# Optimization experiments

Measured on AMD Instinct MI355X. Metric: run time of the kernel, lower is better.

The kernel has to match this reference:

```python
import jax, jax.numpy as jnp
import numpy as np

N = 100000    # nodes
E = 800000    # directed edges
EF = 16       # edge features
NF = 1        # node features (forced by the module's MLP-size constraint)
HID = NF * 8  # NNConv out = 8
H1, C1 = 8, 16  # gat1 heads / per-head channels -> 128
NC = 16       # num_classes (gat2: heads=1, out=NC)


def setup_inputs() -> dict:
    key = jax.random.key(0)
    ks = jax.random.split(key, 20)
    s = 0.1
    return {
        "x": jax.random.normal(ks[0], (N, NF), jnp.float32),
        "edge_index": jax.random.randint(ks[1], (2, E), 0, N, jnp.int64),
        "edge_attr": jax.random.normal(ks[2], (E, EF), jnp.float32),
        # edge MLP: Linear(EF,8) -> ReLU -> Linear(8,8)
        "w1": jax.random.normal(ks[3], (EF, HID), jnp.float32) * s,
        "b1": jnp.zeros((HID,), jnp.float32),
        "w2": jax.random.normal(ks[4], (HID, HID), jnp.float32) * s,
        "b2": jnp.zeros((HID,), jnp.float32),
        # NNConv root weight + bias
        "root": jax.random.normal(ks[5], (NF, HID), jnp.float32) * s,
        "nn_bias": jnp.zeros((HID,), jnp.float32),
        # GAT1: in 8 -> 16 ch x 8 heads
        "g1W": jax.random.normal(ks[6], (HID, H1 * C1), jnp.float32) * s,
        "g1as": jax.random.normal(ks[7], (H1, C1), jnp.float32) * s,
        "g1ad": jax.random.normal(ks[8], (H1, C1), jnp.float32) * s,
        "g1b": jnp.zeros((H1 * C1,), jnp.float32),
        # GAT2: in 128 -> NC, 1 head
        "g2W": jax.random.normal(ks[9], (H1 * C1, NC), jnp.float32) * s,
        "g2as": jax.random.normal(ks[10], (1, NC), jnp.float32) * s,
        "g2ad": jax.random.normal(ks[11], (1, NC), jnp.float32) * s,
        "g2b": jnp.zeros((NC,), jnp.float32),
    }


def _gat(h_in, W, a_src, a_dst, bias, src, dst, n, heads, ch):
    # h: [N, heads, ch]
    h = (h_in @ W).reshape(n, heads, ch)
    e_s = jnp.einsum("nhc,hc->nh", h, a_src)   # per-node src logits
    e_d = jnp.einsum("nhc,hc->nh", h, a_dst)
    e = jax.nn.leaky_relu(e_s[src] + e_d[dst], 0.2)      # [E2, heads]
    m = jax.ops.segment_max(e, dst, num_segments=n)      # segment softmax
    e = jnp.exp(e - m[dst])
    z = jax.ops.segment_sum(e, dst, num_segments=n)
    alpha = e / (z[dst] + 1e-16)                          # [E2, heads]
    out = jax.ops.segment_sum(alpha[:, :, None] * h[src], dst, num_segments=n)
    return out.reshape(n, heads * ch) + bias


def reference(x, edge_index, edge_attr, w1, b1, w2, b2, root, nn_bias,
              g1W, g1as, g1ad, g1b, g2W, g2as, g2ad, g2b):
    n = x.shape[0]
    src, dst = edge_index[0], edge_index[1]

    # ---- NNConv (aggr='mean'): per-edge weight from edge MLP ----
    w_e = jax.nn.relu(edge_attr @ w1 + b1) @ w2 + b2      # [E, NF*HID]
    w_e = w_e.reshape(-1, NF, HID)
    msg = jnp.einsum("ei,eio->eo", x[src], w_e)            # [E, HID]
    sums = jax.ops.segment_sum(msg, dst, num_segments=n)
    cnt = jax.ops.segment_sum(jnp.ones((msg.shape[0],), msg.dtype), dst, num_segments=n)
    aggr = sums / jnp.maximum(cnt, 1.0)[:, None]
    h = jax.nn.relu(aggr + x @ root + nn_bias)             # [N, 8]
    # dropout: eval mode -> identity

    # ---- add self-loops (PyG GATConv default) ----
    loops = jnp.arange(n, dtype=src.dtype)
    src2 = jnp.concatenate([src, loops])
    dst2 = jnp.concatenate([dst, loops])

    h = jax.nn.elu(_gat(h, g1W, g1as, g1ad, g1b, src2, dst2, n, H1, C1))  # [N,128]
    out = _gat(h, g2W, g2as, g2ad, g2b, src2, dst2, n, 1, NC)             # [N,16]
    return jax.nn.log_softmax(out, axis=1)
```

## Files before the change

kernel.cpp:

```cpp
#include <hip/hip_runtime.h>
#include <hip/hip_fp16.h>
#include <math.h>

constexpr int NN  = 100000;
constexpr int NE  = 800000;
constexpr int H1 = 8, C1 = 16;
constexpr int D1 = H1 * C1;
constexpr int NC = 16;
constexpr int SCAN_B = 256;
constexpr int SCAN_NB = (NN + SCAN_B - 1) / SCAN_B;

static inline int cdiv(int a, int b) { return (a + b - 1) / b; }

typedef int   v4i __attribute__((ext_vector_type(4)));

__device__ inline __half2 h2_bits(unsigned u) {
    __half2 r; __builtin_memcpy(&r, &u, 4); return r;
}
__device__ inline __half2 shflx_h2(__half2 v, int off) {
    int iv; __builtin_memcpy(&iv, &v, 4);
    iv = __shfl_xor(iv, off);
    __half2 r; __builtin_memcpy(&r, &iv, 4); return r;
}

__global__ void hist_kernel(const int* __restrict__ dst, int* __restrict__ deg) {
    int e = blockIdx.x * blockDim.x + threadIdx.x;
    if (e < NE) atomicAdd(&deg[dst[e]], 1);
}

__global__ void scan1(const int* __restrict__ deg, int* __restrict__ row,
                      int* __restrict__ partial) {
    __shared__ int s[SCAN_B];
    int tid = threadIdx.x;
    int i = blockIdx.x * SCAN_B + tid;
    int v = (i < NN) ? deg[i] : 0;
    s[tid] = v;
    __syncthreads();
    for (int off = 1; off < SCAN_B; off <<= 1) {
        int t = 0;
        if (tid >= off) t = s[tid - off];
        __syncthreads();
        s[tid] += t;
        __syncthreads();
    }
    if (i < NN) row[i] = s[tid] - v;
    if (tid == SCAN_B - 1) partial[blockIdx.x] = s[tid];
}

__global__ void scan2(int* __restrict__ partial, int nb) {
    __shared__ int s[512];
    int tid = threadIdx.x;
    int v = (tid < nb) ? partial[tid] : 0;
    s[tid] = v;
    __syncthreads();
    for (int off = 1; off < 512; off <<= 1) {
        int t = 0;
        if (tid >= off) t = s[tid - off];
        __syncthreads();
        s[tid] += t;
        __syncthreads();
    }
    if (tid < nb) partial[tid] = s[tid] - v;
}

__global__ void scan3(int* __restrict__ row, const int* __restrict__ partial,
                      int* __restrict__ cursor) {
    int i = blockIdx.x * SCAN_B + threadIdx.x;
    if (i < NN) {
        int r = row[i] + partial[blockIdx.x];
        row[i] = r;
        cursor[i] = r;
    }
}

__global__ void nnconv_scatter(const float* __restrict__ x,
                               const int* __restrict__ src, const int* __restrict__ dst,
                               const float* __restrict__ ea,
                               const float* __restrict__ w1, const float* __restrict__ b1,
                               const float* __restrict__ w2, const float* __restrict__ b2,
                               int* __restrict__ cursor,
                               int* __restrict__ src_s, int* __restrict__ eid_s,
                               __half* __restrict__ msg_s) {
    __shared__ float sw1[16 * 8], sw2[8 * 8], sb1[8], sb2[8];
    int t = threadIdx.x;
    if (t < 128) sw1[t] = w1[t];
    else if (t < 192) sw2[t - 128] = w2[t - 128];
    else if (t < 200) sb1[t - 192] = b1[t - 192];
    else if (t < 208) sb2[t - 200] = b2[t - 200];
    __syncthreads();
    int e = blockIdx.x * blockDim.x + t;
    if (e >= NE) return;

    float a[16];
    const float4* ea4 = (const float4*)(ea + (size_t)e * 16);
    float4 v0 = ea4[0], v1 = ea4[1], v2 = ea4[2], v3 = ea4[3];
    a[0]=v0.x; a[1]=v0.y; a[2]=v0.z; a[3]=v0.w;
    a[4]=v1.x; a[5]=v1.y; a[6]=v1.z; a[7]=v1.w;
    a[8]=v2.x; a[9]=v2.y; a[10]=v2.z; a[11]=v2.w;
    a[12]=v3.x; a[13]=v3.y; a[14]=v3.z; a[15]=v3.w;

    float hdn[8];
#pragma unroll
    for (int j = 0; j < 8; j++) {
        float s = sb1[j];
#pragma unroll
        for (int i = 0; i < 16; i++) s = fmaf(a[i], sw1[i * 8 + j], s);
        hdn[j] = fmaxf(s, 0.f);
    }
    int sn = src[e], dn = dst[e];
    float xv = x[sn];
    __align__(16) __half msg[8];
#pragma unroll
    for (int j = 0; j < 8; j++) {
        float s = sb2[j];
#pragma unroll
        for (int i = 0; i < 8; i++) s = fmaf(hdn[i], sw2[i * 8 + j], s);
        msg[j] = __float2half(xv * s);
    }
    v4i mv; __builtin_memcpy(&mv, msg, 16);
    __builtin_nontemporal_store(mv, (v4i*)(msg_s + (size_t)e * 8));
    int pos = atomicAdd(&cursor[dn], 1);
    src_s[pos] = sn;
    eid_s[pos] = e;
}

__global__ void fused_node1(const float* __restrict__ x,
                            const int* __restrict__ row, const int* __restrict__ deg,
                            const int* __restrict__ eid_s,
                            const __half* __restrict__ msg_s,
                            const float* __restrict__ root, const float* __restrict__ nb,
                            const float* __restrict__ W,
                            const float* __restrict__ as_, const float* __restrict__ ad_,
                            __half* __restrict__ h1h,
                            float* __restrict__ es, float* __restrict__ ed) {
    int t = blockIdx.x * blockDim.x + threadIdx.x;
    if (t >= NN * 8) return;
    int n = t >> 3, j = t & 7;
    int rs = row[n], d = deg[n];

    float p0 = 0.f, p1 = 0.f, p2 = 0.f, p3 = 0.f;
    float p4 = 0.f, p5 = 0.f, p6 = 0.f, p7 = 0.f;
    for (int k = j; k < d; k += 8) {
        int eid = eid_s[rs + k];
        uint4 m = *(const uint4*)(msg_s + (size_t)eid * 8);
        float2 f0 = __half22float2(h2_bits(m.x));
        float2 f1 = __half22float2(h2_bits(m.y));
        float2 f2 = __half22float2(h2_bits(m.z));
        float2 f3 = __half22float2(h2_bits(m.w));
        p0 += f0.x; p1 += f0.y; p2 += f1.x; p3 += f1.y;
        p4 += f2.x; p5 += f2.y; p6 += f3.x; p7 += f3.y;
    }
    float k0 = (j & 4) ? p4 : p0, s0 = (j & 4) ? p0 : p4;
    float k1 = (j & 4) ? p5 : p1, s1 = (j & 4) ? p1 : p5;
    float k2 = (j & 4) ? p6 : p2, s2 = (j & 4) ? p2 : p6;
    float k3 = (j & 4) ? p7 : p3, s3 = (j & 4) ? p3 : p7;
    k0 += __shfl_xor(s0, 4); k1 += __shfl_xor(s1, 4);
    k2 += __shfl_xor(s2, 4); k3 += __shfl_xor(s3, 4);
    float m0 = (j & 2) ? k2 : k0, n0 = (j & 2) ? k0 : k2;
    float m1 = (j & 2) ? k3 : k1, n1 = (j & 2) ? k1 : k3;
    m0 += __shfl_xor(n0, 2); m1 += __shfl_xor(n1, 2);
    float q  = (j & 1) ? m1 : m0, r = (j & 1) ? m0 : m1;
    float sum = q + __shfl_xor(r, 1);

    float hj = fmaxf(sum / fmaxf((float)d, 1.f) + x[n] * root[j] + nb[j], 0.f);

    float hv[8];
#pragma unroll
    for (int k = 0; k < 8; k++) hv[k] = __shfl(hj, k, 8);

    int hd = j;
    float acc[16];
#pragma unroll
    for (int c = 0; c < 16; c++) acc[c] = 0.f;
#pragma unroll
    for (int k = 0; k < 8; k++) {
        const float* wr = W + k * D1 + hd * 16;
#pragma unroll
        for (int c = 0; c < 16; c++) acc[c] = fmaf(hv[k], wr[c], acc[c]);
    }
    float s = 0.f, dd = 0.f;
    __align__(16) __half hh[16];
#pragma unroll
    for (int c = 0; c < 16; c++) {
        s = fmaf(acc[c], as_[hd * 16 + c], s);
        dd = fmaf(acc[c], ad_[hd * 16 + c], dd);
        hh[c] = __float2half(acc[c]);
    }
    float4* hp = (float4*)(h1h + (size_t)n * D1 + hd * 16);
    hp[0] = ((const float4*)hh)[0];
    hp[1] = ((const float4*)hh)[1];
    es[t] = s;
    ed[t] = dd;
}

__global__ __launch_bounds__(256) void gat1_gather(
        const int* __restrict__ row, const int* __restrict__ deg,
        const int* __restrict__ src_s,
        const float* __restrict__ es, const float* __restrict__ ed,
        const __half* __restrict__ h1h, const float* __restrict__ b,
        const float* __restrict__ W2,
        const float* __restrict__ as2, const float* __restrict__ ad2,
        __half* __restrict__ h2h, float* __restrict__ es2, float* __restrict__ ed2) {
    __shared__ float sW2[2048];
    __shared__ float so[4][4][132];
    int tid = threadIdx.x;
    for (int idx = tid; idx < 2048; idx += 256) sW2[idx] = W2[idx];
    __syncthreads();

    int wv = tid >> 6, lane = tid & 63;
    int g  = lane >> 4;
    int cl = lane & 15;
    int hd = cl >> 1;
    const uint4* h1h4 = (const uint4*)h1h;
    float4 bv0 = *((const float4*)(b + cl * 8));
    float4 bv1 = *((const float4*)(b + cl * 8 + 4));

    int base = (blockIdx.x * 4 + wv) * 4;
    for (int i = 0; i < 4; i++) {
        int node = base + i;
        int rs = row[node], d = deg[node];
        float edn = ed[node * 8 + hd];

        float vs = es[node * 8 + hd] + edn;
        vs = fmaxf(vs, 0.2f * vs);
        float a0 = (g == 0) ? __expf(vs) : 0.f;
        float z = a0;
        __half2 ap = __float2half2_rn(a0);
        uint4 gl = h1h4[(unsigned)node * 16u + (unsigned)cl];
        __half2 acc0 = __hmul2(ap, h2_bits(gl.x));
        __half2 acc1 = __hmul2(ap, h2_bits(gl.y));
        __half2 acc2 = __hmul2(ap, h2_bits(gl.z));
        __half2 acc3 = __hmul2(ap, h2_bits(gl.w));

        for (int k = g; k < d; k += 4) {
            int s = src_s[rs + k];
            float v = es[(unsigned)s * 8u + hd] + edn;
            v = fmaxf(v, 0.2f * v);
            float a = __expf(v);
            uint4 ge = h1h4[(unsigned)s * 16u + (unsigned)cl];
            __half2 a2 = __float2half2_rn(a);
            z += a;
            acc0 = __hfma2(a2, h2_bits(ge.x), acc0);
            acc1 = __hfma2(a2, h2_bits(ge.y), acc1);
            acc2 = __hfma2(a2, h2_bits(ge.z), acc2);
            acc3 = __hfma2(a2, h2_bits(ge.w), acc3);
        }
        z += __shfl_xor(z, 16); z += __shfl_xor(z, 32);
        acc0 = __hadd2(acc0, shflx_h2(acc0, 16)); acc0 = __hadd2(acc0, shflx_h2(acc0, 32));
        acc1 = __hadd2(acc1, shflx_h2(acc1, 16)); acc1 = __hadd2(acc1, shflx_h2(acc1, 32));
        acc2 = __hadd2(acc2, shflx_h2(acc2, 16)); acc2 = __hadd2(acc2, shflx_h2(acc2, 32));
        acc3 = __hadd2(acc3, shflx_h2(acc3, 16)); acc3 = __hadd2(acc3, shflx_h2(acc3, 32));

        float rz = 1.f / (z + 1e-16f);
        float2 f0 = __half22float2(acc0), f1 = __half22float2(acc1);
        float2 f2 = __half22float2(acc2), f3 = __half22float2(acc3);
        float o0 = fmaf(f0.x, rz, bv0.x), o1 = fmaf(f0.y, rz, bv0.y);
        float o2 = fmaf(f1.x, rz, bv0.z), o3 = fmaf(f1.y, rz, bv0.w);
        float o4 = fmaf(f2.x, rz, bv1.x), o5 = fmaf(f2.y, rz, bv1.y);
        float o6 = fmaf(f3.x, rz, bv1.z), o7 = fmaf(f3.y, rz, bv1.w);
        o0 = o0 > 0.f ? o0 : __expf(o0) - 1.f;
        o1 = o1 > 0.f ? o1 : __expf(o1) - 1.f;
        o2 = o2 > 0.f ? o2 : __expf(o2) - 1.f;
        o3 = o3 > 0.f ? o3 : __expf(o3) - 1.f;
        o4 = o4 > 0.f ? o4 : __expf(o4) - 1.f;
        o5 = o5 > 0.f ? o5 : __expf(o5) - 1.f;
        o6 = o6 > 0.f ? o6 : __expf(o6) - 1.f;
        o7 = o7 > 0.f ? o7 : __expf(o7) - 1.f;
        if (g == 0) {
            float4* sp = (float4*)&so[wv][i][cl * 8];
            sp[0] = make_float4(o0, o1, o2, o3);
            sp[1] = make_float4(o4, o5, o6, o7);
        }
    }
    __asm__ __volatile__("s_waitcnt lgkmcnt(0)" ::: "memory");

    int nl = lane >> 4, c = lane & 15;
    float partial = 0.f;
#pragma unroll 4
    for (int k = 0; k < 128; k += 2) {
        float2 sv = *(const float2*)&so[wv][nl][k];
        partial = fmaf(sv.x, sW2[k * 16 + c], partial);
        partial = fmaf(sv.y, sW2[(k + 1) * 16 + c], partial);
    }
    float ta = partial * as2[c], tb = partial * ad2[c];
#pragma unroll
    for (int off = 1; off < 16; off <<= 1) {
        ta += __shfl_xor(ta, off);
        tb += __shfl_xor(tb, off);
    }
    h2h[(size_t)(base + nl) * 16 + c] = __float2half(partial);
    if (c == 0) { es2[base + nl] = ta; ed2[base + nl] = tb; }
}

__global__ __launch_bounds__(256) void gat2_gather(
        const int* __restrict__ row, const int* __restrict__ deg,
        const int* __restrict__ src_s,
        const float* __restrict__ es, const float* __restrict__ ed,
        const __half* __restrict__ h2h, const float* __restrict__ b,
        float* __restrict__ out) {
    int tid = threadIdx.x;
    int wv = tid >> 6, lane = tid & 63;
    int g = lane >> 3, l = lane & 7;
    const unsigned* h2i = (const unsigned*)h2h;
    float2 bv = ((const float2*)b)[l];
    int base = (blockIdx.x * 4 + wv) * 4;
    for (int i = 0; i < 4; i++) {
        int node = base + i;
        int rs = row[node], d = deg[node];
        float edn = ed[node];
        float vs = es[node] + edn;
        vs = fmaxf(vs, 0.2f * vs);
        float a0 = (g == 0) ? __expf(vs) : 0.f;
        float z = a0;
        __half2 acc = __hmul2(__float2half2_rn(a0),
                              h2_bits(h2i[(unsigned)node * 8u + l]));

        for (int k = g; k < d; k += 8) {
            int s = src_s[rs + k];
            float v = es[s] + edn;
            v = fmaxf(v, 0.2f * v);
            float a = __expf(v);
            unsigned hraw = h2i[(unsigned)s * 8u + l];
            z += a;
            acc = __hfma2(__float2half2_rn(a), h2_bits(hraw), acc);
        }
        z += __shfl_xor(z, 8); z += __shfl_xor(z, 16); z += __shfl_xor(z, 32);
        acc = __hadd2(acc, shflx_h2(acc, 8));
        acc = __hadd2(acc, shflx_h2(acc, 16));
        acc = __hadd2(acc, shflx_h2(acc, 32));

        float rz = 1.f / (z + 1e-16f);
        float2 f = __half22float2(acc);
        float o0 = fmaf(f.x, rz, bv.x);
        float o1 = fmaf(f.y, rz, bv.y);
        float mx = fmaxf(o0, o1);
        mx = fmaxf(mx, __shfl_xor(mx, 1));
        mx = fmaxf(mx, __shfl_xor(mx, 2));
        mx = fmaxf(mx, __shfl_xor(mx, 4));
        float ss = __expf(o0 - mx) + __expf(o1 - mx);
        ss += __shfl_xor(ss, 1); ss += __shfl_xor(ss, 2); ss += __shfl_xor(ss, 4);
        float lg = mx + __logf(ss);
        if (g == 0)
            ((float2*)out)[(unsigned)node * 8u + l] = make_float2(o0 - lg, o1 - lg);
    }
}

extern "C" void kernel_launch(void* const* d_in, const int* in_sizes, int n_in,
                              void* d_out, int out_size, void* d_ws, size_t ws_size,
                              hipStream_t stream) {
    const float* x    = (const float*)d_in[0];
    const int*   ei   = (const int*)d_in[1];
    const float* ea   = (const float*)d_in[2];
    const float* w1   = (const float*)d_in[3];
    const float* b1   = (const float*)d_in[4];
    const float* w2   = (const float*)d_in[5];
    const float* b2   = (const float*)d_in[6];
    const float* root = (const float*)d_in[7];
    const float* nb   = (const float*)d_in[8];
    const float* g1W  = (const float*)d_in[9];
    const float* g1as = (const float*)d_in[10];
    const float* g1ad = (const float*)d_in[11];
    const float* g1b  = (const float*)d_in[12];
    const float* g2W  = (const float*)d_in[13];
    const float* g2as = (const float*)d_in[14];
    const float* g2ad = (const float*)d_in[15];
    const float* g2b  = (const float*)d_in[16];
    float* out = (float*)d_out;

    const int* src = ei;
    const int* dst = ei + NE;

    float* ws = (float*)d_ws;
    size_t o = 0;
    __half* msg_s  = (__half*)(ws + o); o += (size_t)NE * 4;
    __half* h1h    = (__half*)(ws + o); o += (size_t)NN * D1 / 2;
    __half* h2h    = (__half*)(ws + o); o += (size_t)NN * NC / 2;
    int*  src_s = (int*)(ws + o); o += NE;
    int*  eid_s = (int*)(ws + o); o += NE;
    int*  deg   = (int*)(ws + o); o += NN;
    int*  row   = (int*)(ws + o); o += NN;
    int*  cur   = (int*)(ws + o); o += NN;
    int*  part  = (int*)(ws + o); o += 512;
    float* es1  = ws + o; o += (size_t)NN * H1;
    float* ed1  = ws + o; o += (size_t)NN * H1;
    float* es2  = ws + o; o += NN;
    float* ed2  = ws + o; o += NN;
    (void)ws_size; (void)in_sizes; (void)n_in; (void)out_size;

    const int B = 256;

    hipMemsetAsync(deg, 0, (size_t)NN * sizeof(int), stream);
    hist_kernel<<<cdiv(NE, B), B, 0, stream>>>(dst, deg);
    scan1<<<SCAN_NB, SCAN_B, 0, stream>>>(deg, row, part);
    scan2<<<1, 512, 0, stream>>>(part, SCAN_NB);
    scan3<<<SCAN_NB, SCAN_B, 0, stream>>>(row, part, cur);

    nnconv_scatter<<<cdiv(NE, B), B, 0, stream>>>(x, src, dst, ea, w1, b1, w2, b2,
                                                  cur, src_s, eid_s, msg_s);
    fused_node1<<<cdiv(NN * 8, B), B, 0, stream>>>(x, row, deg, eid_s, msg_s, root, nb,
                                                   g1W, g1as, g1ad, h1h, es1, ed1);
    gat1_gather<<<NN / 16, B, 0, stream>>>(row, deg, src_s, es1, ed1, h1h,
                                           g1b, g2W, g2as, g2ad, h2h, es2, ed2);
    gat2_gather<<<NN / 16, B, 0, stream>>>(row, deg, src_s, es2, ed2, h2h, g2b, out);
}
```

Before: 351.1 us.

## Store GAT1 features as scaled FP8 and scatter messages directly into CSR order

The node features h1 are now stored as FP8 (pre-scaled by 16) instead of FP16, which halves the bytes each edge gather reads in gat1_gather. Accumulation there moves from half2 FMAs to fp32 FMAs. NNConv messages are now written at their sorted CSR position rather than by edge id, which removes the eid_s array and the indirect lookup in fused_node1. In exchange the features lose precision, which may hurt accuracy, and the message stores become scattered instead of coalesced.

```diff
diff --git a/kernel.cpp b/kernel.cpp
--- a/kernel.cpp
+++ b/kernel.cpp
@@ -13,6 +13,7 @@
 static inline int cdiv(int a, int b) { return (a + b - 1) / b; }
 
 typedef int   v4i __attribute__((ext_vector_type(4)));
+typedef float v2f __attribute__((ext_vector_type(2)));
 
 __device__ inline __half2 h2_bits(unsigned u) {
     __half2 r; __builtin_memcpy(&r, &u, 4); return r;
@@ -79,8 +80,7 @@
                                const float* __restrict__ w1, const float* __restrict__ b1,
                                const float* __restrict__ w2, const float* __restrict__ b2,
                                int* __restrict__ cursor,
-                               int* __restrict__ src_s, int* __restrict__ eid_s,
-                               __half* __restrict__ msg_s) {
+                               int* __restrict__ src_s, __half* __restrict__ msg_s) {
     __shared__ float sw1[16 * 8], sw2[8 * 8], sb1[8], sb2[8];
     int t = threadIdx.x;
     if (t < 128) sw1[t] = w1[t];
@@ -117,21 +117,19 @@
         for (int i = 0; i < 8; i++) s = fmaf(hdn[i], sw2[i * 8 + j], s);
         msg[j] = __float2half(xv * s);
     }
+    int pos = atomicAdd(&cursor[dn], 1);
     v4i mv; __builtin_memcpy(&mv, msg, 16);
-    __builtin_nontemporal_store(mv, (v4i*)(msg_s + (size_t)e * 8));
-    int pos = atomicAdd(&cursor[dn], 1);
+    __builtin_nontemporal_store(mv, (v4i*)(msg_s + (size_t)pos * 8));
     src_s[pos] = sn;
-    eid_s[pos] = e;
 }
 
 __global__ void fused_node1(const float* __restrict__ x,
                             const int* __restrict__ row, const int* __restrict__ deg,
-                            const int* __restrict__ eid_s,
                             const __half* __restrict__ msg_s,
                             const float* __restrict__ root, const float* __restrict__ nb,
                             const float* __restrict__ W,
                             const float* __restrict__ as_, const float* __restrict__ ad_,
-                            __half* __restrict__ h1h,
+                            unsigned char* __restrict__ h1f8,
                             float* __restrict__ es, float* __restrict__ ed) {
     int t = blockIdx.x * blockDim.x + threadIdx.x;
     if (t >= NN * 8) return;
@@ -141,8 +139,7 @@
     float p0 = 0.f, p1 = 0.f, p2 = 0.f, p3 = 0.f;
     float p4 = 0.f, p5 = 0.f, p6 = 0.f, p7 = 0.f;
     for (int k = j; k < d; k += 8) {
-        int eid = eid_s[rs + k];
-        uint4 m = *(const uint4*)(msg_s + (size_t)eid * 8);
+        uint4 m = *(const uint4*)(msg_s + (size_t)(rs + k) * 8);
         float2 f0 = __half22float2(h2_bits(m.x));
         float2 f1 = __half22float2(h2_bits(m.y));
         float2 f2 = __half22float2(h2_bits(m.z));
@@ -179,16 +176,19 @@
         for (int c = 0; c < 16; c++) acc[c] = fmaf(hv[k], wr[c], acc[c]);
     }
     float s = 0.f, dd = 0.f;
-    __align__(16) __half hh[16];
 #pragma unroll
     for (int c = 0; c < 16; c++) {
         s = fmaf(acc[c], as_[hd * 16 + c], s);
         dd = fmaf(acc[c], ad_[hd * 16 + c], dd);
-        hh[c] = __float2half(acc[c]);
-    }
-    float4* hp = (float4*)(h1h + (size_t)n * D1 + hd * 16);
-    hp[0] = ((const float4*)hh)[0];
-    hp[1] = ((const float4*)hh)[1];
+    }
+    v4i pk;
+#pragma unroll
+    for (int w = 0; w < 4; w++) {
+        int wd = __builtin_amdgcn_cvt_pk_fp8_f32(acc[4*w] * 16.f, acc[4*w+1] * 16.f, 0, false);
+        wd = __builtin_amdgcn_cvt_pk_fp8_f32(acc[4*w+2] * 16.f, acc[4*w+3] * 16.f, wd, true);
+        pk[w] = wd;
+    }
+    *(v4i*)(h1f8 + (size_t)n * 128 + hd * 16) = pk;
     es[t] = s;
     ed[t] = dd;
 }
@@ -197,7 +197,7 @@
         const int* __restrict__ row, const int* __restrict__ deg,
         const int* __restrict__ src_s,
         const float* __restrict__ es, const float* __restrict__ ed,
-        const __half* __restrict__ h1h, const float* __restrict__ b,
+        const unsigned char* __restrict__ h1f8, const float* __restrict__ b,
         const float* __restrict__ W2,
         const float* __restrict__ as2, const float* __restrict__ ad2,
         __half* __restrict__ h2h, float* __restrict__ es2, float* __restrict__ ed2) {
@@ -211,7 +211,6 @@
     int g  = lane >> 4;
     int cl = lane & 15;
     int hd = cl >> 1;
-    const uint4* h1h4 = (const uint4*)h1h;
     float4 bv0 = *((const float4*)(b + cl * 8));
     float4 bv1 = *((const float4*)(b + cl * 8 + 4));
 
@@ -225,39 +224,45 @@
         vs = fmaxf(vs, 0.2f * vs);
         float a0 = (g == 0) ? __expf(vs) : 0.f;
         float z = a0;
-        __half2 ap = __float2half2_rn(a0);
-        uint4 gl = h1h4[(unsigned)node * 16u + (unsigned)cl];
-        __half2 acc0 = __hmul2(ap, h2_bits(gl.x));
-        __half2 acc1 = __hmul2(ap, h2_bits(gl.y));
-        __half2 acc2 = __hmul2(ap, h2_bits(gl.z));
-        __half2 acc3 = __hmul2(ap, h2_bits(gl.w));
+        uint2 gl = *(const uint2*)(h1f8 + (size_t)node * 128 + cl * 8);
+        v2f d0 = __builtin_amdgcn_cvt_pk_f32_fp8(gl.x, false);
+        v2f d1 = __builtin_amdgcn_cvt_pk_f32_fp8(gl.x, true);
+        v2f d2 = __builtin_amdgcn_cvt_pk_f32_fp8(gl.y, false);
+        v2f d3 = __builtin_amdgcn_cvt_pk_f32_fp8(gl.y, true);
+        float c0 = a0 * d0[0], c1 = a0 * d0[1], c2 = a0 * d1[0], c3 = a0 * d1[1];
+        float c4 = a0 * d2[0], c5 = a0 * d2[1], c6 = a0 * d3[0], c7 = a0 * d3[1];
 
         for (int k = g; k < d; k += 4) {
             int s = src_s[rs + k];
             float v = es[(unsigned)s * 8u + hd] + edn;
             v = fmaxf(v, 0.2f * v);
             float a = __expf(v);
-            uint4 ge = h1h4[(unsigned)s * 16u + (unsigned)cl];
-            __half2 a2 = __float2half2_rn(a);
+            uint2 ge = *(const uint2*)(h1f8 + (size_t)s * 128 + cl * 8);
+            v2f e0 = __builtin_amdgcn_cvt_pk_f32_fp8(ge.x, false);
+            v2f e1 = __builtin_amdgcn_cvt_pk_f32_fp8(ge.x, true);
+            v2f e2 = __builtin_amdgcn_cvt_pk_f32_fp8(ge.y, false);
+            v2f e3 = __builtin_amdgcn_cvt_pk_f32_fp8(ge.y, true);
             z += a;
-            acc0 = __hfma2(a2, h2_bits(ge.x), acc0);
-            acc1 = __hfma2(a2, h2_bits(ge.y), acc1);
-            acc2 = __hfma2(a2, h2_bits(ge.z), acc2);
-            acc3 = __hfma2(a2, h2_bits(ge.w), acc3);
+            c0 = fmaf(a, e0[0], c0); c1 = fmaf(a, e0[1], c1);
+            c2 = fmaf(a, e1[0], c2); c3 = fmaf(a, e1[1], c3);
+            c4 = fmaf(a, e2[0], c4); c5 = fmaf(a, e2[1], c5);
+            c6 = fmaf(a, e3[0], c6); c7 = fmaf(a, e3[1], c7);
         }
         z += __shfl_xor(z, 16); z += __shfl_xor(z, 32);
-        acc0 = __hadd2(acc0, shflx_h2(acc0, 16)); acc0 = __hadd2(acc0, shflx_h2(acc0, 32));
-        acc1 = __hadd2(acc1, shflx_h2(acc1, 16)); acc1 = __hadd2(acc1, shflx_h2(acc1, 32));
-        acc2 = __hadd2(acc2, shflx_h2(acc2, 16)); acc2 = __hadd2(acc2, shflx_h2(acc2, 32));
-        acc3 = __hadd2(acc3, shflx_h2(acc3, 16)); acc3 = __hadd2(acc3, shflx_h2(acc3, 32));
-
-        float rz = 1.f / (z + 1e-16f);
-        float2 f0 = __half22float2(acc0), f1 = __half22float2(acc1);
-        float2 f2 = __half22float2(acc2), f3 = __half22float2(acc3);
-        float o0 = fmaf(f0.x, rz, bv0.x), o1 = fmaf(f0.y, rz, bv0.y);
-        float o2 = fmaf(f1.x, rz, bv0.z), o3 = fmaf(f1.y, rz, bv0.w);
-        float o4 = fmaf(f2.x, rz, bv1.x), o5 = fmaf(f2.y, rz, bv1.y);
-        float o6 = fmaf(f3.x, rz, bv1.z), o7 = fmaf(f3.y, rz, bv1.w);
+        c0 += __shfl_xor(c0, 16); c0 += __shfl_xor(c0, 32);
+        c1 += __shfl_xor(c1, 16); c1 += __shfl_xor(c1, 32);
+        c2 += __shfl_xor(c2, 16); c2 += __shfl_xor(c2, 32);
+        c3 += __shfl_xor(c3, 16); c3 += __shfl_xor(c3, 32);
+        c4 += __shfl_xor(c4, 16); c4 += __shfl_xor(c4, 32);
+        c5 += __shfl_xor(c5, 16); c5 += __shfl_xor(c5, 32);
+        c6 += __shfl_xor(c6, 16); c6 += __shfl_xor(c6, 32);
+        c7 += __shfl_xor(c7, 16); c7 += __shfl_xor(c7, 32);
+
+        float rz = 1.f / (16.f * (z + 1e-16f));
+        float o0 = fmaf(c0, rz, bv0.x), o1 = fmaf(c1, rz, bv0.y);
+        float o2 = fmaf(c2, rz, bv0.z), o3 = fmaf(c3, rz, bv0.w);
+        float o4 = fmaf(c4, rz, bv1.x), o5 = fmaf(c5, rz, bv1.y);
+        float o6 = fmaf(c6, rz, bv1.z), o7 = fmaf(c7, rz, bv1.w);
         o0 = o0 > 0.f ? o0 : __expf(o0) - 1.f;
         o1 = o1 > 0.f ? o1 : __expf(o1) - 1.f;
         o2 = o2 > 0.f ? o2 : __expf(o2) - 1.f;
@@ -373,10 +378,9 @@
     float* ws = (float*)d_ws;
     size_t o = 0;
     __half* msg_s  = (__half*)(ws + o); o += (size_t)NE * 4;
-    __half* h1h    = (__half*)(ws + o); o += (size_t)NN * D1 / 2;
+    unsigned char* h1f8 = (unsigned char*)(ws + o); o += (size_t)NN * 32;
     __half* h2h    = (__half*)(ws + o); o += (size_t)NN * NC / 2;
     int*  src_s = (int*)(ws + o); o += NE;
-    int*  eid_s = (int*)(ws + o); o += NE;
     int*  deg   = (int*)(ws + o); o += NN;
     int*  row   = (int*)(ws + o); o += NN;
     int*  cur   = (int*)(ws + o); o += NN;
@@ -396,10 +400,10 @@
     scan3<<<SCAN_NB, SCAN_B, 0, stream>>>(row, part, cur);
 
     nnconv_scatter<<<cdiv(NE, B), B, 0, stream>>>(x, src, dst, ea, w1, b1, w2, b2,
-                                                  cur, src_s, eid_s, msg_s);
-    fused_node1<<<cdiv(NN * 8, B), B, 0, stream>>>(x, row, deg, eid_s, msg_s, root, nb,
-                                                   g1W, g1as, g1ad, h1h, es1, ed1);
-    gat1_gather<<<NN / 16, B, 0, stream>>>(row, deg, src_s, es1, ed1, h1h,
+                                                  cur, src_s, msg_s);
+    fused_node1<<<cdiv(NN * 8, B), B, 0, stream>>>(x, row, deg, msg_s, root, nb,
+                                                   g1W, g1as, g1ad, h1f8, es1, ed1);
+    gat1_gather<<<NN / 16, B, 0, stream>>>(row, deg, src_s, es1, ed1, h1f8,
                                            g1b, g2W, g2as, g2ad, h2h, es2, ed2);
     gat2_gather<<<NN / 16, B, 0, stream>>>(row, deg, src_s, es2, ed2, h2h, g2b, out);
 }
```

Result: faster. 328.5 us (-6.4%).
